# Kernel tuning notes

Measured on AMD Instinct MI355X. Metric: run time of the kernel, lower is better.

## Reference

```python
import jax, jax.numpy as jnp
import numpy as np

B, S, HID = 1, 2048, 3072
NH, NKV, HD = 24, 8, 128
ROT = 96
OP = NH * HD + 2 * NKV * HD
MASK_VALUE = -jnp.finfo(jnp.float32).max


def setup_inputs() -> dict:
    key = jax.random.key(0)
    k1, k2, k3, k4, k5 = jax.random.split(key, 5)
    hidden_states = jax.random.normal(k1, (B, S, HID), dtype=jnp.float32)
    # rotary embeddings: use actual cos/sin of rope angles for realism
    inv_freq = 1.0 / (10000.0 ** (jnp.arange(0, ROT, 2, dtype=jnp.float32) / ROT))
    t = jnp.arange(S, dtype=jnp.float32)
    freqs = jnp.outer(t, inv_freq)  # [S, ROT/2]
    emb = jnp.concatenate([freqs, freqs], axis=-1)  # [S, ROT]
    cos = jnp.broadcast_to(jnp.cos(emb)[None], (B, S, ROT))
    sin = jnp.broadcast_to(jnp.sin(emb)[None], (B, S, ROT))
    attention_mask = jnp.ones((B, S), dtype=bool)
    w_qkv = jax.random.normal(k2, (OP, HID), dtype=jnp.float32) * (HID ** -0.5)
    w_o = jax.random.normal(k3, (HID, HID), dtype=jnp.float32) * (HID ** -0.5)
    return {"hidden_states": hidden_states, "cos": cos, "sin": sin,
            "attention_mask": attention_mask, "w_qkv": w_qkv, "w_o": w_o}


def rotate_half(x):
    x1, x2 = jnp.split(x, 2, axis=-1)
    return jnp.concatenate([-x2, x1], axis=-1)


def apply_rope(q, k, cos, sin):
    # cos/sin: [B, S, ROT] -> [B, 1, S, ROT]
    cos = cos[:, None]
    sin = sin[:, None]
    rd = cos.shape[-1]
    q_rot, q_pass = q[..., :rd], q[..., rd:]
    k_rot, k_pass = k[..., :rd], k[..., rd:]
    q = jnp.concatenate([q_rot * cos + rotate_half(q_rot) * sin, q_pass], axis=-1)
    k = jnp.concatenate([k_rot * cos + rotate_half(k_rot) * sin, k_pass], axis=-1)
    return q, k


def reference(hidden_states, cos, sin, attention_mask, w_qkv, w_o):
    b, n, _ = hidden_states.shape
    qkv = hidden_states @ w_qkv.T  # [B, S, OP]
    q, k, v = jnp.split(qkv, [NH * HD, NH * HD + NKV * HD], axis=-1)
    # b n (h d) -> b h n d
    q = q.reshape(b, n, NH, HD).transpose(0, 2, 1, 3)
    k = k.reshape(b, n, NKV, HD).transpose(0, 2, 1, 3)
    v = v.reshape(b, n, NKV, HD).transpose(0, 2, 1, 3)
    q, k = apply_rope(q, k, cos, sin)
    q = q * (HD ** -0.5)
    n_rep = NH // NKV
    if n_rep > 1:
        k = jnp.repeat(k, n_rep, axis=1)
        v = jnp.repeat(v, n_rep, axis=1)
    sim = jnp.einsum('bhid,bhjd->bhij', q, k)
    causal = jnp.triu(jnp.ones((n, n), dtype=bool), k=1)
    sim = jnp.where(causal, MASK_VALUE, sim)
    sim = jnp.where(~attention_mask[:, None, None, :], MASK_VALUE, sim)
    attn = jax.nn.softmax(sim.astype(jnp.float32), axis=-1).astype(v.dtype)
    out = jnp.einsum('bhij,bhjd->bhid', attn, v)
    out = out.transpose(0, 2, 1, 3).reshape(b, n, NH * HD)  # b h n d -> b n (h d)
    return out @ w_o.T
```

## Files before the change

### kernel.cpp

```cpp
#include <hip/hip_runtime.h>

typedef unsigned short u16;
typedef unsigned int u32;
typedef __bf16 bf16x8 __attribute__((ext_vector_type(8)));
typedef float f32x4 __attribute__((ext_vector_type(4)));

#define S_LEN 2048
#define HIDDEN 3072
#define NHEADS 24
#define NKVH 8
#define HDIM 128
#define QKVW 5120
#define QKLD 4096
#define PSTR 80

__device__ __forceinline__ u16 f2bf(float f) {
  u32 u = __float_as_uint(f);
  u32 r = (u + 0x7fffu + ((u >> 16) & 1u)) >> 16;
  return (u16)r;
}
__device__ __forceinline__ float bf2f(u16 h) { return __uint_as_float(((u32)h) << 16); }

__device__ __forceinline__ void gload_lds16(const void* g, void* l) {
  __builtin_amdgcn_global_load_lds((const __attribute__((address_space(1))) void*)g,
                                   (__attribute__((address_space(3))) void*)l, 16, 0, 0);
}

__global__ void cast4(const float4* __restrict__ in, uint2* __restrict__ out, int n4) {
  int i = blockIdx.x * blockDim.x + threadIdx.x;
  if (i >= n4) return;
  float4 f = in[i];
  uint2 o;
  o.x = ((u32)f2bf(f.y) << 16) | f2bf(f.x);
  o.y = ((u32)f2bf(f.w) << 16) | f2bf(f.z);
  out[i] = o;
}

__global__ __launch_bounds__(512, 2) void gemm256(const u16* __restrict__ A,
                                                  const u16* __restrict__ B,
                                                  u16* __restrict__ Cb,
                                                  u16* __restrict__ vtg) {
  __shared__ u16 lds[4][13312];
  const int tid = threadIdx.x;
  const int w = tid >> 6, lane = tid & 63;
  const int wm = w & 3, wn = w >> 2;
  const int l15 = lane & 15, qd = lane >> 4;
  const int K = 3072;
  const int m0 = ((int)blockIdx.x & 7) * 256;
  const int n0 = ((int)blockIdx.x >> 3) * 160;

  size_t offA[2], offB[2];
  int ldsA[2], ldsB[2];
#pragma unroll
  for (int it = 0; it < 2; ++it) {
    int CH = w * 128 + it * 64 + lane;
    int rp = CH >> 3, sl = CH & 7;
    int lin = sl ^ (rp & 7);
    int r = (rp << 1) | (lin >> 2), q = lin & 3;
    offA[it] = (size_t)(m0 + r) * K + q * 8;
    ldsA[it] = (w * 128 + it * 64) * 8;
  }
#pragma unroll
  for (int it = 0; it < 2; ++it) {
    int CH = it * 512 + w * 64 + lane;
    int rp = CH >> 3, sl = CH & 7;
    int lin = sl ^ (rp & 7);
    int r = (rp << 1) | (lin >> 2), q = lin & 3;
    offB[it] = (size_t)(n0 + r) * K + q * 8;
    ldsB[it] = 8192 + (it * 512 + w * 64) * 8;
  }

  int chA[4], chB[5];
#pragma unroll
  for (int i = 0; i < 4; ++i) {
    int r = wm * 64 + i * 16 + l15;
    chA[i] = ((r >> 1) * 8 + ((((r & 1) << 2) | qd) ^ ((r >> 1) & 7))) * 8;
  }
#pragma unroll
  for (int j = 0; j < 5; ++j) {
    int r = wn * 80 + j * 16 + l15;
    chB[j] = 8192 + ((r >> 1) * 8 + ((((r & 1) << 2) | qd) ^ ((r >> 1) & 7))) * 8;
  }

  f32x4 acc[4][5] = {};

  auto stage = [&](int s, int k0) {
    gload_lds16(A + offA[0] + k0, &lds[s][ldsA[0]]);
    gload_lds16(A + offA[1] + k0, &lds[s][ldsA[1]]);
    gload_lds16(B + offB[0] + k0, &lds[s][ldsB[0]]);
    if (w < 2) gload_lds16(B + offB[1] + k0, &lds[s][ldsB[1]]);
  };

  auto tile = [&](int s, int kpf, bool pf) {
    if (pf) stage((kpf >> 5) & 3, kpf);
    bf16x8 a[4], b[5];
#pragma unroll
    for (int i = 0; i < 4; ++i) a[i] = *(const bf16x8*)&lds[s][chA[i]];
#pragma unroll
    for (int j = 0; j < 5; ++j) b[j] = *(const bf16x8*)&lds[s][chB[j]];
    __builtin_amdgcn_s_setprio(1);
#pragma unroll
    for (int i = 0; i < 4; ++i)
#pragma unroll
      for (int j = 0; j < 5; ++j)
        acc[i][j] = __builtin_amdgcn_mfma_f32_16x16x32_bf16(a[i], b[j], acc[i][j], 0, 0, 0);
    __builtin_amdgcn_s_setprio(0);
  };

  stage(0, 0);
  stage(1, 32);
  stage(2, 64);
  if (w < 2) asm volatile("s_waitcnt vmcnt(8)" ::: "memory");
  else       asm volatile("s_waitcnt vmcnt(6)" ::: "memory");
  __builtin_amdgcn_s_barrier();

  for (int t = 0; t < 93; ++t) {
    tile(t & 3, (t + 3) * 32, true);
    if (w < 2) asm volatile("s_waitcnt vmcnt(8)" ::: "memory");
    else       asm volatile("s_waitcnt vmcnt(6)" ::: "memory");
    __builtin_amdgcn_s_barrier();
  }
  tile(1, 0, false);
  if (w < 2) asm volatile("s_waitcnt vmcnt(4)" ::: "memory");
  else       asm volatile("s_waitcnt vmcnt(3)" ::: "memory");
  __builtin_amdgcn_s_barrier();
  tile(2, 0, false);
  asm volatile("s_waitcnt vmcnt(0)" ::: "memory");
  __builtin_amdgcn_s_barrier();
  tile(3, 0, false);

#pragma unroll
  for (int j = 0; j < 5; ++j) {
    const int nf = n0 + wn * 80 + j * 16;
    if (nf >= 4096) {
#pragma unroll
      for (int i = 0; i < 4; ++i) {
        int nv = nf - 4096 + l15;
        int m = m0 + wm * 64 + i * 16 + qd * 4;
        uint2 p;
        p.x = ((u32)f2bf(acc[i][j][1]) << 16) | f2bf(acc[i][j][0]);
        p.y = ((u32)f2bf(acc[i][j][3]) << 16) | f2bf(acc[i][j][2]);
        *(uint2*)&vtg[(size_t)nv * S_LEN + m] = p;
      }
    } else {
#pragma unroll
      for (int i = 0; i < 4; ++i)
#pragma unroll
        for (int r = 0; r < 4; ++r) {
          int m = m0 + wm * 64 + i * 16 + qd * 4 + r;
          Cb[(size_t)m * QKLD + nf + l15] = f2bf(acc[i][j][r]);
        }
    }
  }
}

__global__ __launch_bounds__(512, 2) void gemm2k(const u16* __restrict__ A,
                                                 const u16* __restrict__ B,
                                                 float* __restrict__ C) {
  __shared__ u16 lds[4][10240];
  const int tid = threadIdx.x;
  const int w = tid >> 6, lane = tid & 63;
  const int wm = w & 1, wn = w >> 1;
  const int l15 = lane & 15, qd = lane >> 4;
  const int K = 3072;
  const int xcd = (int)blockIdx.x & 7, idx = (int)blockIdx.x >> 3;
  const int m0 = ((xcd & 1) * 8 + (idx & 7)) * 128;
  const int n0 = ((xcd >> 1) * 4 + (idx >> 3)) * 192;

  size_t offA, offB[2];
  int ldsAo, ldsB[2];
  {
    int CH = w * 64 + lane;
    int rp = CH >> 3, sl = CH & 7;
    int lin = sl ^ (rp & 7);
    int r = (rp << 1) | (lin >> 2), q = lin & 3;
    offA = (size_t)(m0 + r) * K + q * 8;
    ldsAo = (w * 64) * 8;
  }
#pragma unroll
  for (int it = 0; it < 2; ++it) {
    int CHb = (w < 4) ? (w * 128 + it * 64) : (512 + (w - 4) * 64);
    int CH = CHb + lane;
    int rp = CH >> 3, sl = CH & 7;
    int lin = sl ^ (rp & 7);
    int r = (rp << 1) | (lin >> 2), q = lin & 3;
    offB[it] = (size_t)(n0 + r) * K + q * 8;
    ldsB[it] = 4096 + CHb * 8;
  }

  int chA[4], chB[3];
#pragma unroll
  for (int i = 0; i < 4; ++i) {
    int r = wm * 64 + i * 16 + l15;
    chA[i] = ((r >> 1) * 8 + ((((r & 1) << 2) | qd) ^ ((r >> 1) & 7))) * 8;
  }
#pragma unroll
  for (int j = 0; j < 3; ++j) {
    int r = wn * 48 + j * 16 + l15;
    chB[j] = 4096 + ((r >> 1) * 8 + ((((r & 1) << 2) | qd) ^ ((r >> 1) & 7))) * 8;
  }

  f32x4 acc[4][3] = {};

  auto stage = [&](int s, int k0) {
    gload_lds16(A + offA + k0, &lds[s][ldsAo]);
    gload_lds16(B + offB[0] + k0, &lds[s][ldsB[0]]);
    if (w < 4) gload_lds16(B + offB[1] + k0, &lds[s][ldsB[1]]);
  };

  auto tile = [&](int s, int kpf, bool pf) {
    if (pf) stage((kpf >> 5) & 3, kpf);
    bf16x8 a[4], b[3];
#pragma unroll
    for (int i = 0; i < 4; ++i) a[i] = *(const bf16x8*)&lds[s][chA[i]];
#pragma unroll
    for (int j = 0; j < 3; ++j) b[j] = *(const bf16x8*)&lds[s][chB[j]];
    __builtin_amdgcn_s_setprio(1);
#pragma unroll
    for (int i = 0; i < 4; ++i)
#pragma unroll
      for (int j = 0; j < 3; ++j)
        acc[i][j] = __builtin_amdgcn_mfma_f32_16x16x32_bf16(a[i], b[j], acc[i][j], 0, 0, 0);
    __builtin_amdgcn_s_setprio(0);
  };

  stage(0, 0);
  stage(1, 32);
  stage(2, 64);
  if (w < 4) asm volatile("s_waitcnt vmcnt(6)" ::: "memory");
  else       asm volatile("s_waitcnt vmcnt(4)" ::: "memory");
  __builtin_amdgcn_s_barrier();

  for (int t = 0; t < 93; ++t) {
    tile(t & 3, (t + 3) * 32, true);
    if (w < 4) asm volatile("s_waitcnt vmcnt(6)" ::: "memory");
    else       asm volatile("s_waitcnt vmcnt(4)" ::: "memory");
    __builtin_amdgcn_s_barrier();
  }
  tile(1, 0, false);
  if (w < 4) asm volatile("s_waitcnt vmcnt(3)" ::: "memory");
  else       asm volatile("s_waitcnt vmcnt(2)" ::: "memory");
  __builtin_amdgcn_s_barrier();
  tile(2, 0, false);
  asm volatile("s_waitcnt vmcnt(0)" ::: "memory");
  __builtin_amdgcn_s_barrier();
  tile(3, 0, false);

#pragma unroll
  for (int i = 0; i < 4; ++i)
#pragma unroll
    for (int j = 0; j < 3; ++j)
#pragma unroll
      for (int r = 0; r < 4; ++r) {
        int m = m0 + wm * 64 + i * 16 + qd * 4 + r;
        int n = n0 + wn * 48 + j * 16 + l15;
        C[(size_t)m * HIDDEN + n] = acc[i][j][r];
      }
}

__global__ __launch_bounds__(128) void rope_kernel(u16* __restrict__ qkv,
                                                   const float* __restrict__ cosb,
                                                   const float* __restrict__ sinb) {
  const int s = blockIdx.x;
  const int hh = blockIdx.y;
  const int d = threadIdx.x;
  const bool isq = hh < NHEADS;
  const size_t base = (size_t)s * QKLD + (isq ? hh * HDIM : HIDDEN + (hh - NHEADS) * HDIM);
  const float scale = 0.08838834764831845f;
  if (d < 48) {
    float x1 = bf2f(qkv[base + d]), x2 = bf2f(qkv[base + d + 48]);
    float c1 = cosb[s * 96 + d], s1 = sinb[s * 96 + d];
    float c2 = cosb[s * 96 + d + 48], s2 = sinb[s * 96 + d + 48];
    float o1 = x1 * c1 - x2 * s1;
    float o2 = x2 * c2 + x1 * s2;
    if (isq) { o1 *= scale; o2 *= scale; }
    qkv[base + d] = f2bf(o1);
    qkv[base + d + 48] = f2bf(o2);
  } else if (d >= 96 && isq) {
    qkv[base + d] = f2bf(bf2f(qkv[base + d]) * scale);
  }
}

__global__ __launch_bounds__(256) void flash_kernel(const u16* __restrict__ qkv,
                                                    const u16* __restrict__ vtg,
                                                    u16* __restrict__ ao) {
  __shared__ u16 Ks[4][64 * 32];
  __shared__ u16 Vt[128 * PSTR];
  __shared__ u16 Ps[64 * PSTR];
  const int bid = blockIdx.x;
  const int g = bid & 255, kk3 = bid >> 8;
  const int rank = (kk3 == 1) ? (kk3 << 8) + (255 - g) : (kk3 << 8) + g;
  const int h = rank % NHEADS;
  const int qi = 31 - rank / NHEADS;
  const int q0 = qi * 64;
  const int hkv = h / 3;
  const int tid = threadIdx.x;
  const int w = tid >> 6, lane = tid & 63;
  const int l15 = lane & 15, qd = lane >> 4;
  const int rS = lane >> 2, cS = (lane & 3) * 8;

  bf16x8 qf[4];
#pragma unroll
  for (int kk = 0; kk < 4; ++kk)
    qf[kk] = *(const bf16x8*)&qkv[(size_t)(q0 + w * 16 + l15) * QKLD + h * HDIM + kk * 32 + qd * 8];

  f32x4 o[8] = {};
  float lrow[4] = {0.f, 0.f, 0.f, 0.f};

  const u16* vb = vtg + (size_t)hkv * HDIM * S_LEN;
  const int vd = tid >> 3;
  const int vkv = (tid & 7) * 8;

  for (int kv0 = 0; kv0 <= q0; kv0 += 64) {
    __syncthreads();
#pragma unroll
    for (int t = 0; t < 4; ++t)
      gload_lds16(qkv + (size_t)(kv0 + t * 16 + rS) * QKLD + HIDDEN + hkv * HDIM + w * 32 + cS,
                  &Ks[w][t * 16 * 32]);
#pragma unroll
    for (int it = 0; it < 4; ++it) {
      int d = it * 32 + vd;
      uint4 vv = *(const uint4*)&vb[(size_t)d * S_LEN + kv0 + vkv];
      *(uint4*)&Vt[d * PSTR + vkv] = vv;
    }
    __syncthreads();

    f32x4 sc[4] = {};
#pragma unroll
    for (int j = 0; j < 4; ++j)
#pragma unroll
      for (int kk = 0; kk < 4; ++kk) {
        bf16x8 kf = *(const bf16x8*)&Ks[kk][(j * 16 + l15) * 32 + qd * 8];
        sc[j] = __builtin_amdgcn_mfma_f32_16x16x32_bf16(qf[kk], kf, sc[j], 0, 0, 0);
      }

    if (kv0 == q0) {
#pragma unroll
      for (int j = 0; j < 4; ++j)
#pragma unroll
        for (int r = 0; r < 4; ++r) {
          int row = w * 16 + qd * 4 + r;
          int col = j * 16 + l15;
          if (col > row) sc[j][r] = -1.0e30f;
        }
    }

#pragma unroll
    for (int j = 0; j < 4; ++j)
#pragma unroll
      for (int r = 0; r < 4; ++r) sc[j][r] = __expf(sc[j][r]);
#pragma unroll
    for (int r = 0; r < 4; ++r)
      lrow[r] += (sc[0][r] + sc[1][r]) + (sc[2][r] + sc[3][r]);

#pragma unroll
    for (int j = 0; j < 4; ++j)
#pragma unroll
      for (int r = 0; r < 4; ++r)
        Ps[(w * 16 + qd * 4 + r) * PSTR + j * 16 + l15] = f2bf(sc[j][r]);
    asm volatile("s_waitcnt lgkmcnt(0)" ::: "memory");

    bf16x8 pf[2];
#pragma unroll
    for (int kk = 0; kk < 2; ++kk)
      pf[kk] = *(const bf16x8*)&Ps[(w * 16 + l15) * PSTR + kk * 32 + qd * 8];
#pragma unroll
    for (int jn = 0; jn < 8; ++jn)
#pragma unroll
      for (int kk = 0; kk < 2; ++kk) {
        bf16x8 vf = *(const bf16x8*)&Vt[(jn * 16 + l15) * PSTR + kk * 32 + qd * 8];
        o[jn] = __builtin_amdgcn_mfma_f32_16x16x32_bf16(pf[kk], vf, o[jn], 0, 0, 0);
      }
  }

  float rinv[4];
#pragma unroll
  for (int r = 0; r < 4; ++r) {
    float s = lrow[r];
#pragma unroll
    for (int d = 1; d < 16; d <<= 1) s += __shfl_xor(s, d, 64);
    rinv[r] = 1.0f / s;
  }
#pragma unroll
  for (int jn = 0; jn < 8; ++jn)
#pragma unroll
    for (int r = 0; r < 4; ++r) {
      int row = q0 + w * 16 + qd * 4 + r;
      ao[(size_t)row * HIDDEN + h * HDIM + jn * 16 + l15] = f2bf(o[jn][r] * rinv[r]);
    }
}

extern "C" void kernel_launch(void* const* d_in, const int* in_sizes, int n_in,
                              void* d_out, int out_size, void* d_ws, size_t ws_size,
                              hipStream_t stream) {
  (void)in_sizes; (void)n_in; (void)out_size; (void)ws_size;
  const float* hs   = (const float*)d_in[0];
  const float* cosb = (const float*)d_in[1];
  const float* sinb = (const float*)d_in[2];
  const float* wqkv = (const float*)d_in[4];
  const float* wo   = (const float*)d_in[5];
  float* out = (float*)d_out;
  char* ws = (char*)d_ws;

  u16* hB   = (u16*)ws;
  u16* wB   = (u16*)(ws + 12582912);
  u16* qkvB = (u16*)(ws + 44040192);
  u16* vtgB = (u16*)(ws + 60817408);
  u16* aoB  = hB;
  u16* woB  = wB;

  cast4<<<6144, 256, 0, stream>>>((const float4*)hs, (uint2*)hB, 1572864);
  cast4<<<15360, 256, 0, stream>>>((const float4*)wqkv, (uint2*)wB, 3932160);
  gemm256<<<256, 512, 0, stream>>>(hB, wB, qkvB, vtgB);
  cast4<<<9216, 256, 0, stream>>>((const float4*)wo, (uint2*)woB, 2359296);
  rope_kernel<<<dim3(2048, 32), 128, 0, stream>>>(qkvB, cosb, sinb);
  flash_kernel<<<768, 256, 0, stream>>>(qkvB, vtgB, aoB);
  gemm2k<<<256, 512, 0, stream>>>(aoB, woB, out);
}
```

Before: 347.4 us.

## Deepen GEMM LDS pipeline to five stages and double-buffer register fragments

Both bf16 GEMM kernels (QKV and output projection) now keep five LDS stages instead of four, with four tiles prefetched before the main loop. The loop is unrolled by two and alternates two register fragment sets: the next tile's LDS reads are issued while the current tile's MFMAs run, with a sched_barrier keeping them ordered. The aim is to hide global-to-LDS and LDS-to-register latency behind matrix math. In exchange, LDS use per block grows, occupancy stays at one block per CU, and register pressure rises from the duplicated fragments.

```diff
diff --git a/kernel.cpp b/kernel.cpp
--- a/kernel.cpp
+++ b/kernel.cpp
@@ -40,7 +40,7 @@
                                                   const u16* __restrict__ B,
                                                   u16* __restrict__ Cb,
                                                   u16* __restrict__ vtg) {
-  __shared__ u16 lds[4][13312];
+  __shared__ u16 lds[5][13312];
   const int tid = threadIdx.x;
   const int w = tid >> 6, lane = tid & 63;
   const int wm = w & 3, wn = w >> 2;
@@ -90,44 +90,61 @@
     gload_lds16(B + offB[0] + k0, &lds[s][ldsB[0]]);
     if (w < 2) gload_lds16(B + offB[1] + k0, &lds[s][ldsB[1]]);
   };
-
-  auto tile = [&](int s, int kpf, bool pf) {
-    if (pf) stage((kpf >> 5) & 3, kpf);
-    bf16x8 a[4], b[5];
-#pragma unroll
-    for (int i = 0; i < 4; ++i) a[i] = *(const bf16x8*)&lds[s][chA[i]];
-#pragma unroll
-    for (int j = 0; j < 5; ++j) b[j] = *(const bf16x8*)&lds[s][chB[j]];
+  auto rdf = [&](int s, bf16x8 (&Af)[4], bf16x8 (&Bf)[5]) {
+#pragma unroll
+    for (int i = 0; i < 4; ++i) Af[i] = *(const bf16x8*)&lds[s][chA[i]];
+#pragma unroll
+    for (int j = 0; j < 5; ++j) Bf[j] = *(const bf16x8*)&lds[s][chB[j]];
+  };
+  auto mm = [&](bf16x8 (&Af)[4], bf16x8 (&Bf)[5]) {
+    __builtin_amdgcn_sched_barrier(0);
     __builtin_amdgcn_s_setprio(1);
 #pragma unroll
     for (int i = 0; i < 4; ++i)
 #pragma unroll
       for (int j = 0; j < 5; ++j)
-        acc[i][j] = __builtin_amdgcn_mfma_f32_16x16x32_bf16(a[i], b[j], acc[i][j], 0, 0, 0);
+        acc[i][j] = __builtin_amdgcn_mfma_f32_16x16x32_bf16(Af[i], Bf[j], acc[i][j], 0, 0, 0);
     __builtin_amdgcn_s_setprio(0);
   };
 
   stage(0, 0);
   stage(1, 32);
   stage(2, 64);
+  stage(3, 96);
   if (w < 2) asm volatile("s_waitcnt vmcnt(8)" ::: "memory");
   else       asm volatile("s_waitcnt vmcnt(6)" ::: "memory");
   __builtin_amdgcn_s_barrier();
 
-  for (int t = 0; t < 93; ++t) {
-    tile(t & 3, (t + 3) * 32, true);
+  bf16x8 A0[4], B0[5], A1[4], B1[5];
+  rdf(0, A0, B0);
+
+  int sp = 4, sc = 1;
+  for (int t = 0; t < 92; t += 2) {
+    stage(sp, (t + 4) * 32); sp = (sp == 4) ? 0 : sp + 1;
+    rdf(sc, A1, B1);         sc = (sc == 4) ? 0 : sc + 1;
+    mm(A0, B0);
     if (w < 2) asm volatile("s_waitcnt vmcnt(8)" ::: "memory");
     else       asm volatile("s_waitcnt vmcnt(6)" ::: "memory");
     __builtin_amdgcn_s_barrier();
-  }
-  tile(1, 0, false);
+    stage(sp, (t + 5) * 32); sp = (sp == 4) ? 0 : sp + 1;
+    rdf(sc, A0, B0);         sc = (sc == 4) ? 0 : sc + 1;
+    mm(A1, B1);
+    if (w < 2) asm volatile("s_waitcnt vmcnt(8)" ::: "memory");
+    else       asm volatile("s_waitcnt vmcnt(6)" ::: "memory");
+    __builtin_amdgcn_s_barrier();
+  }
+  rdf(3, A1, B1);
+  mm(A0, B0);
   if (w < 2) asm volatile("s_waitcnt vmcnt(4)" ::: "memory");
   else       asm volatile("s_waitcnt vmcnt(3)" ::: "memory");
   __builtin_amdgcn_s_barrier();
-  tile(2, 0, false);
+  rdf(4, A0, B0);
+  mm(A1, B1);
   asm volatile("s_waitcnt vmcnt(0)" ::: "memory");
   __builtin_amdgcn_s_barrier();
-  tile(3, 0, false);
+  rdf(0, A1, B1);
+  mm(A0, B0);
+  mm(A1, B1);
 
 #pragma unroll
   for (int j = 0; j < 5; ++j) {
@@ -157,7 +174,7 @@
 __global__ __launch_bounds__(512, 2) void gemm2k(const u16* __restrict__ A,
                                                  const u16* __restrict__ B,
                                                  float* __restrict__ C) {
-  __shared__ u16 lds[4][10240];
+  __shared__ u16 lds[5][10240];
   const int tid = threadIdx.x;
   const int w = tid >> 6, lane = tid & 63;
   const int wm = w & 1, wn = w >> 1;
@@ -207,44 +224,61 @@
     gload_lds16(B + offB[0] + k0, &lds[s][ldsB[0]]);
     if (w < 4) gload_lds16(B + offB[1] + k0, &lds[s][ldsB[1]]);
   };
-
-  auto tile = [&](int s, int kpf, bool pf) {
-    if (pf) stage((kpf >> 5) & 3, kpf);
-    bf16x8 a[4], b[3];
-#pragma unroll
-    for (int i = 0; i < 4; ++i) a[i] = *(const bf16x8*)&lds[s][chA[i]];
-#pragma unroll
-    for (int j = 0; j < 3; ++j) b[j] = *(const bf16x8*)&lds[s][chB[j]];
+  auto rdf = [&](int s, bf16x8 (&Af)[4], bf16x8 (&Bf)[3]) {
+#pragma unroll
+    for (int i = 0; i < 4; ++i) Af[i] = *(const bf16x8*)&lds[s][chA[i]];
+#pragma unroll
+    for (int j = 0; j < 3; ++j) Bf[j] = *(const bf16x8*)&lds[s][chB[j]];
+  };
+  auto mm = [&](bf16x8 (&Af)[4], bf16x8 (&Bf)[3]) {
+    __builtin_amdgcn_sched_barrier(0);
     __builtin_amdgcn_s_setprio(1);
 #pragma unroll
     for (int i = 0; i < 4; ++i)
 #pragma unroll
       for (int j = 0; j < 3; ++j)
-        acc[i][j] = __builtin_amdgcn_mfma_f32_16x16x32_bf16(a[i], b[j], acc[i][j], 0, 0, 0);
+        acc[i][j] = __builtin_amdgcn_mfma_f32_16x16x32_bf16(Af[i], Bf[j], acc[i][j], 0, 0, 0);
     __builtin_amdgcn_s_setprio(0);
   };
 
   stage(0, 0);
   stage(1, 32);
   stage(2, 64);
+  stage(3, 96);
   if (w < 4) asm volatile("s_waitcnt vmcnt(6)" ::: "memory");
   else       asm volatile("s_waitcnt vmcnt(4)" ::: "memory");
   __builtin_amdgcn_s_barrier();
 
-  for (int t = 0; t < 93; ++t) {
-    tile(t & 3, (t + 3) * 32, true);
+  bf16x8 A0[4], B0[3], A1[4], B1[3];
+  rdf(0, A0, B0);
+
+  int sp = 4, sc = 1;
+  for (int t = 0; t < 92; t += 2) {
+    stage(sp, (t + 4) * 32); sp = (sp == 4) ? 0 : sp + 1;
+    rdf(sc, A1, B1);         sc = (sc == 4) ? 0 : sc + 1;
+    mm(A0, B0);
     if (w < 4) asm volatile("s_waitcnt vmcnt(6)" ::: "memory");
     else       asm volatile("s_waitcnt vmcnt(4)" ::: "memory");
     __builtin_amdgcn_s_barrier();
-  }
-  tile(1, 0, false);
+    stage(sp, (t + 5) * 32); sp = (sp == 4) ? 0 : sp + 1;
+    rdf(sc, A0, B0);         sc = (sc == 4) ? 0 : sc + 1;
+    mm(A1, B1);
+    if (w < 4) asm volatile("s_waitcnt vmcnt(6)" ::: "memory");
+    else       asm volatile("s_waitcnt vmcnt(4)" ::: "memory");
+    __builtin_amdgcn_s_barrier();
+  }
+  rdf(3, A1, B1);
+  mm(A0, B0);
   if (w < 4) asm volatile("s_waitcnt vmcnt(3)" ::: "memory");
   else       asm volatile("s_waitcnt vmcnt(2)" ::: "memory");
   __builtin_amdgcn_s_barrier();
-  tile(2, 0, false);
+  rdf(4, A0, B0);
+  mm(A1, B1);
   asm volatile("s_waitcnt vmcnt(0)" ::: "memory");
   __builtin_amdgcn_s_barrier();
-  tile(3, 0, false);
+  rdf(0, A1, B1);
+  mm(A0, B0);
+  mm(A1, B1);
 
 #pragma unroll
   for (int i = 0; i < 4; ++i)
```

After: 353.1 us. No clear change (+1.6%).

## Double-buffer K tiles and prefetch V into registers in flash kernel

Applied to the files above, without the earlier changes.

Splits the K shared-memory tile into two buffers and issues the async global-to-LDS load for the next K tile while the current tile's QK^T MFMAs run. The next V tile is loaded into registers during compute and written to the transposed LDS buffer at the start of the following iteration. The barrier pattern is reorganized around this: a vmcnt wait plus barrier at loop top, and a barrier after the P writes. The aim is to hide global memory latency behind MFMA work, at the cost of more LDS and registers, which may reduce occupancy.

```diff
diff --git a/kernel.cpp b/kernel.cpp
--- a/kernel.cpp
+++ b/kernel.cpp
@@ -284,7 +284,7 @@
 __global__ __launch_bounds__(256) void flash_kernel(const u16* __restrict__ qkv,
                                                     const u16* __restrict__ vtg,
                                                     u16* __restrict__ ao) {
-  __shared__ u16 Ks[4][64 * 32];
+  __shared__ u16 Ks[2][4][64 * 32];
   __shared__ u16 Vt[128 * PSTR];
   __shared__ u16 Ps[64 * PSTR];
   const int bid = blockIdx.x;
@@ -311,28 +311,43 @@
   const int vd = tid >> 3;
   const int vkv = (tid & 7) * 8;
 
-  for (int kv0 = 0; kv0 <= q0; kv0 += 64) {
-    __syncthreads();
+  auto stageK = [&](int b, int kv0) {
 #pragma unroll
     for (int t = 0; t < 4; ++t)
       gload_lds16(qkv + (size_t)(kv0 + t * 16 + rS) * QKLD + HIDDEN + hkv * HDIM + w * 32 + cS,
-                  &Ks[w][t * 16 * 32]);
-#pragma unroll
-    for (int it = 0; it < 4; ++it) {
-      int d = it * 32 + vd;
-      uint4 vv = *(const uint4*)&vb[(size_t)d * S_LEN + kv0 + vkv];
-      *(uint4*)&Vt[d * PSTR + vkv] = vv;
-    }
-    __syncthreads();
+                  &Ks[b][w][t * 16 * 32]);
+  };
+  uint4 vv[4];
+  auto loadV = [&](int kv0) {
+#pragma unroll
+    for (int it = 0; it < 4; ++it)
+      vv[it] = *(const uint4*)&vb[(size_t)(it * 32 + vd) * S_LEN + kv0 + vkv];
+  };
+
+  stageK(0, 0);
+  loadV(0);
+
+  int buf = 0;
+  for (int kv0 = 0; kv0 <= q0; kv0 += 64) {
+    asm volatile("s_waitcnt vmcnt(0)\n\ts_barrier" ::: "memory");
+
+#pragma unroll
+    for (int it = 0; it < 4; ++it)
+      *(uint4*)&Vt[(it * 32 + vd) * PSTR + vkv] = vv[it];
+
+    const bool pfn = (kv0 + 64 <= q0);
+    if (pfn) stageK(buf ^ 1, kv0 + 64);
 
     f32x4 sc[4] = {};
 #pragma unroll
     for (int j = 0; j < 4; ++j)
 #pragma unroll
       for (int kk = 0; kk < 4; ++kk) {
-        bf16x8 kf = *(const bf16x8*)&Ks[kk][(j * 16 + l15) * 32 + qd * 8];
+        bf16x8 kf = *(const bf16x8*)&Ks[buf][kk][(j * 16 + l15) * 32 + qd * 8];
         sc[j] = __builtin_amdgcn_mfma_f32_16x16x32_bf16(qf[kk], kf, sc[j], 0, 0, 0);
       }
+
+    if (pfn) loadV(kv0 + 64);
 
     if (kv0 == q0) {
 #pragma unroll
@@ -358,7 +373,8 @@
 #pragma unroll
       for (int r = 0; r < 4; ++r)
         Ps[(w * 16 + qd * 4 + r) * PSTR + j * 16 + l15] = f2bf(sc[j][r]);
-    asm volatile("s_waitcnt lgkmcnt(0)" ::: "memory");
+
+    asm volatile("s_waitcnt lgkmcnt(0)\n\ts_barrier" ::: "memory");
 
     bf16x8 pf[2];
 #pragma unroll
@@ -371,6 +387,7 @@
         bf16x8 vf = *(const bf16x8*)&Vt[(jn * 16 + l15) * PSTR + kk * 32 + qd * 8];
         o[jn] = __builtin_amdgcn_mfma_f32_16x16x32_bf16(pf[kk], vf, o[jn], 0, 0, 0);
       }
+    buf ^= 1;
   }
 
   float rinv[4];
```

Result: slower. 374.9 us (+7.9%).
